# Performance work log

Measured on AMD Instinct MI355X. Metric: run time of the kernel, lower is better.

The kernel has to match this reference:

```python
import jax, jax.numpy as jnp
import numpy as np

B, D, E, H, OUT = 4096, 1024, 8, 4096, 1024


def setup_inputs() -> dict:
    key = jax.random.key(0)
    ks = jax.random.split(key, 8)
    s_in = 1.0 / np.sqrt(D)
    s_h = 1.0 / np.sqrt(H)
    return {
        "x": jax.random.normal(ks[0], (B, D), dtype=jnp.float32),
        "Wg": jax.random.uniform(ks[1], (D, E), minval=-s_in, maxval=s_in, dtype=jnp.float32),
        "bg": jnp.zeros((E,), dtype=jnp.float32),
        "W1": jax.random.uniform(ks[2], (E, D, H), minval=-s_in, maxval=s_in, dtype=jnp.float32),
        "b1": jnp.zeros((E, H), dtype=jnp.float32),
        "W2": jax.random.uniform(ks[3], (E, H, OUT), minval=-s_h, maxval=s_h, dtype=jnp.float32),
        "b2": jnp.zeros((E, OUT), dtype=jnp.float32),
        "w_bal": jnp.float32(0.01),
    }


def reference(x, Wg, bg, W1, b1, W2, b2, w_bal):
    # Gating: softmax then top-1 (== argmax of logits)
    gate_logits = x @ Wg + bg                      # [B, E]
    assign = jnp.argmax(gate_logits, axis=1)       # [B] top-1 expert
    onehot = jax.nn.one_hot(assign, E, dtype=x.dtype)  # [B, E] dispatch mask

    # Dense dispatch: run every expert MLP, combine by one-hot (top-1 select).
    # Original returns raw expert output (no gate-prob scaling).
    h = jax.nn.relu(jnp.einsum("bd,edh->ebh", x, W1) + b1[:, None, :])  # [E, B, H]
    y = jnp.einsum("ebh,eho->ebo", h, W2) + b2[:, None, :]              # [E, B, OUT]
    output = jnp.einsum("ebo,be->bo", y, onehot)                        # [B, OUT]

    # Load-balance loss on per-expert token counts
    loads = onehot.sum(axis=0)                     # [E]
    balance_loss = jnp.sum((loads - loads.mean()) ** 2) / E
    return output, balance_loss * w_bal
```

## Files before the change

kernel.cpp:

```cpp
#include <hip/hip_runtime.h>
#include <hip/hip_bf16.h>

typedef unsigned short u16;
typedef __attribute__((ext_vector_type(8))) short bf16x8;
typedef __attribute__((ext_vector_type(4))) float f32x4;

#define BTOK 4096
#define DDIM 1024
#define NEXP 8
#define HDIM 4096
#define ODIM 1024
#define MAXT 23
#define MROWS (MAXT * 256)

__device__ __forceinline__ u16 f2bf(float f) {
  unsigned u = __float_as_uint(f);
  return (u16)((u + 0x7FFFu + ((u >> 16) & 1u)) >> 16);
}
__device__ __forceinline__ u16 cvt_bf(float f) {
  __hip_bfloat16 h = __float2bfloat16(f);
  u16 r;
  __builtin_memcpy(&r, &h, 2);
  return r;
}

__device__ __forceinline__ void gload16(const void* g, void* l) {
  __builtin_amdgcn_global_load_lds(
      (const __attribute__((address_space(1))) void*)g,
      (__attribute__((address_space(3))) void*)l, 16, 0, 0);
}

__global__ __launch_bounds__(256) void init_kernel(int* __restrict__ ctrl,
                                                   int* __restrict__ rowmap) {
  int i = blockIdx.x * 256 + threadIdx.x;
  if (i < 1024)
    ctrl[i] = 0;
  else
    rowmap[i - 1024] = -1;
}

__global__ __launch_bounds__(256) void gate_kernel(
    const float* __restrict__ x, const float* __restrict__ Wg,
    const float* __restrict__ bg, int* __restrict__ assign,
    int* __restrict__ counts) {
  int wave = threadIdx.x >> 6;
  int lane = threadIdx.x & 63;
  int b = blockIdx.x * 4 + wave;
  const float* xr = x + (size_t)b * DDIM;
  double acc[NEXP];
#pragma unroll
  for (int e = 0; e < NEXP; ++e) acc[e] = 0.0;
  for (int d = lane; d < DDIM; d += 64) {
    float xv = xr[d];
    const float4* wrow = (const float4*)(Wg + d * NEXP);
    float4 w0 = wrow[0], w1 = wrow[1];
    acc[0] += (double)xv * (double)w0.x;
    acc[1] += (double)xv * (double)w0.y;
    acc[2] += (double)xv * (double)w0.z;
    acc[3] += (double)xv * (double)w0.w;
    acc[4] += (double)xv * (double)w1.x;
    acc[5] += (double)xv * (double)w1.y;
    acc[6] += (double)xv * (double)w1.z;
    acc[7] += (double)xv * (double)w1.w;
  }
#pragma unroll
  for (int e = 0; e < NEXP; ++e) {
    double v = acc[e];
#pragma unroll
    for (int off = 32; off > 0; off >>= 1) v += __shfl_xor(v, off);
    acc[e] = v;
  }
  if (lane == 0) {
    int best = 0;
    double bv = acc[0] + (double)bg[0];
#pragma unroll
    for (int e = 1; e < NEXP; ++e) {
      double v = acc[e] + (double)bg[e];
      if (v > bv) { bv = v; best = e; }
    }
    assign[b] = best;
    atomicAdd(&counts[best], 1);
  }
}

__global__ void setup_kernel(const int* __restrict__ counts,
                             const float* __restrict__ wbal,
                             int* __restrict__ offp, int* __restrict__ tile_e,
                             int* __restrict__ tile_m, int* __restrict__ meta,
                             float* __restrict__ loss_out) {
  if (threadIdx.x != 0 || blockIdx.x != 0) return;
  int off = 0, nt = 0;
  for (int e = 0; e < NEXP; ++e) {
    offp[e] = off;
    int pc = (counts[e] + 255) & ~255;
    for (int t = 0; t < (pc >> 8); ++t) {
      tile_e[nt] = e;
      tile_m[nt] = off + t * 256;
      ++nt;
    }
    off += pc;
  }
  offp[NEXP] = off;
  meta[0] = nt;
  float mean = (float)BTOK / (float)NEXP;
  float s = 0.f;
  for (int e = 0; e < NEXP; ++e) {
    float d = (float)counts[e] - mean;
    s += d * d;
  }
  loss_out[0] = s / (float)NEXP * wbal[0];
}

__global__ __launch_bounds__(256) void gather_kernel(
    const float* __restrict__ x, const int* __restrict__ assign,
    const int* __restrict__ offp, int* __restrict__ fill,
    int* __restrict__ rowmap, u16* __restrict__ xg) {
  int b = blockIdx.x;
  __shared__ int srow;
  if (threadIdx.x == 0) {
    int e = assign[b];
    int pos = atomicAdd(&fill[e], 1);
    int row = offp[e] + pos;
    rowmap[row] = b;
    srow = row;
  }
  __syncthreads();
  int row = srow;
  float4 v = *(const float4*)(x + (size_t)b * DDIM + threadIdx.x * 4);
  ushort4 o;
  o.x = f2bf(v.x);
  o.y = f2bf(v.y);
  o.z = f2bf(v.z);
  o.w = f2bf(v.w);
  *(ushort4*)(xg + (size_t)row * DDIM + threadIdx.x * 4) = o;
}

__global__ __launch_bounds__(256) void transpose_conv(
    const float* __restrict__ W, u16* __restrict__ wt, int N, int K) {
  const int e = blockIdx.z;
  const int kb = blockIdx.x * 128, nb = blockIdx.y * 64;
  __shared__ __align__(16) float lds[128][68];
  const float* src = W + (size_t)e * K * N;
  const int t = threadIdx.x;
  const int rr = t >> 4, cc = (t & 15) * 4;
#pragma unroll
  for (int p = 0; p < 8; ++p) {
    float4 v =
        *(const float4*)(src + (size_t)(kb + rr + p * 16) * N + nb + cc);
    *(float4*)&lds[rr + p * 16][cc] = v;
  }
  __syncthreads();
  const int n = t & 63, ks = (t >> 6) * 32;
  alignas(16) u16 tmp[32];
#pragma unroll
  for (int i = 0; i < 32; ++i) tmp[i] = cvt_bf(lds[ks + i][n]);
  u16* dst = wt + ((size_t)e * N + nb + n) * K + kb + ks;
  *(float4*)dst = *(float4*)&tmp[0];
  *(float4*)(dst + 8) = *(float4*)&tmp[8];
  *(float4*)(dst + 16) = *(float4*)&tmp[16];
  *(float4*)(dst + 24) = *(float4*)&tmp[24];
}

template <int MODE>
__device__ __forceinline__ void gemm_core(
    u16* lds, int bx, int by, int bz, const u16* __restrict__ A, int lda,
    const u16* __restrict__ BT, int ldb, int nbRows,
    const float* __restrict__ bias, const int* __restrict__ tile_e,
    const int* __restrict__ tile_m, u16* __restrict__ Hout, int ldn,
    float* __restrict__ P, size_t pStride, int nkt) {
  const int e = tile_e[bx];
  const int m0 = tile_m[bx];
  const int n0 = by * 128;
  const int kOff = bz * nkt * 32;

  const int tid = threadIdx.x;
  const int lane = tid & 63;
  const int wave = tid >> 6;
  const int wr = wave >> 1, wc = wave & 1;
  const int fr = lane & 15;
  const int kqr = lane >> 4;

  const int r0 = tid >> 2, k0 = (tid & 3) ^ ((r0 >> 1) & 3);
  const int r1 = (tid + 512) >> 2, k1 = ((tid + 512) & 3) ^ ((r1 >> 1) & 3);
  const u16* aS0 = A + (size_t)(m0 + r0) * lda + kOff + k0 * 8;
  const u16* aS1 = A + (size_t)(m0 + r1) * lda + kOff + k1 * 8;
  const u16* bPan = BT + ((size_t)e * nbRows + n0) * ldb + kOff;
  const u16* bS0 = bPan + (size_t)r0 * ldb + k0 * 8;
  const int dstA0 = (tid & ~63) * 8;
  const int dstA1 = dstA0 + 512 * 8;
  const int dstB = (tid & ~63) * 8;

  int aOff[4], bOff[4];
#pragma unroll
  for (int i = 0; i < 4; ++i) {
    int r = wr * 64 + i * 16 + fr;
    aOff[i] = (r * 4 + (kqr ^ ((r >> 1) & 3))) * 8;
    int c = wc * 64 + i * 16 + fr;
    bOff[i] = 8192 + (c * 4 + (kqr ^ ((c >> 1) & 3))) * 8;
  }

  f32x4 acc[4][4];
#pragma unroll
  for (int i = 0; i < 4; ++i)
#pragma unroll
    for (int j = 0; j < 4; ++j)
#pragma unroll
      for (int r = 0; r < 4; ++r) acc[i][j][r] = 0.f;

  auto stage = [&](int buf, int kt) {
    const int ko = kt * 32;
    u16* base = lds + buf * 12288;
    gload16(aS0 + ko, base + dstA0);
    gload16(aS1 + ko, base + dstA1);
    gload16(bS0 + ko, base + 8192 + dstB);
  };
  auto compute = [&](int buf) {
    const u16* base = lds + buf * 12288;
    bf16x8 af[4], bfr[4];
#pragma unroll
    for (int i = 0; i < 4; ++i) {
      af[i] = *(const bf16x8*)(base + aOff[i]);
      bfr[i] = *(const bf16x8*)(base + bOff[i]);
    }
    __builtin_amdgcn_s_setprio(1);
#pragma unroll
    for (int i = 0; i < 4; ++i)
#pragma unroll
      for (int j = 0; j < 4; ++j)
        acc[i][j] = __builtin_amdgcn_mfma_f32_16x16x32_bf16(af[i], bfr[j],
                                                            acc[i][j], 0, 0, 0);
    __builtin_amdgcn_s_setprio(0);
  };

  stage(0, 0);
  stage(1, 1);
  __builtin_amdgcn_sched_barrier(0);
  asm volatile("s_waitcnt vmcnt(3)" ::: "memory");
  __builtin_amdgcn_s_barrier();
  __builtin_amdgcn_sched_barrier(0);

  int cur = 0, nst = 2;
#pragma unroll 1
  for (int t = 0; t < nkt; ++t) {
    const bool more = (t + 2 < nkt);
    if (more) stage(nst, t + 2);
    compute(cur);
    cur = (cur == 2) ? 0 : cur + 1;
    nst = (nst == 2) ? 0 : nst + 1;
    if (t + 1 < nkt) {
      __builtin_amdgcn_sched_barrier(0);
      if (more)
        asm volatile("s_waitcnt vmcnt(3)" ::: "memory");
      else
        asm volatile("s_waitcnt vmcnt(0)" ::: "memory");
      __builtin_amdgcn_s_barrier();
      __builtin_amdgcn_sched_barrier(0);
    }
  }

  if constexpr (MODE == 0) {
#pragma unroll
    for (int i = 0; i < 4; ++i) {
      int rbase = m0 + wr * 64 + i * 16 + (lane >> 4) * 4;
#pragma unroll
      for (int j = 0; j < 4; ++j) {
        int col = n0 + wc * 64 + j * 16 + fr;
        float bv = bias[e * ldn + col];
#pragma unroll
        for (int r = 0; r < 4; ++r) {
          float v = acc[i][j][r] + bv;
          v = v > 0.f ? v : 0.f;
          Hout[(size_t)(rbase + r) * ldn + col] = f2bf(v);
        }
      }
    }
  } else {
    float* Pp = P + bz * pStride;
#pragma unroll
    for (int i = 0; i < 4; ++i) {
      int rbase = m0 + wr * 64 + i * 16 + (lane >> 4) * 4;
#pragma unroll
      for (int j = 0; j < 4; ++j) {
        int col = n0 + wc * 64 + j * 16 + fr;
#pragma unroll
        for (int r = 0; r < 4; ++r)
          Pp[(size_t)(rbase + r) * ODIM + col] = acc[i][j][r];
      }
    }
  }
}

__global__ __launch_bounds__(512, 4) void moe_gemm1(
    const u16* __restrict__ xg, const u16* __restrict__ wt1,
    const float* __restrict__ b1, const int* __restrict__ tile_e,
    const int* __restrict__ tile_m, const int* __restrict__ meta,
    u16* __restrict__ h) {
  __shared__ __align__(16) u16 lds[3 * 12288];
  const int orig = blockIdx.y * MAXT + blockIdx.x;
  const int xcd = orig & 7;
  const int i = orig >> 3;
  const int bx = i >> 2;
  const int by = xcd * 4 + (i & 3);
  if (bx >= meta[0]) return;
  gemm_core<0>(lds, bx, by, 0, xg, DDIM, wt1, DDIM, HDIM, b1, tile_e, tile_m,
               h, HDIM, nullptr, 0, DDIM / 32);
}

__global__ __launch_bounds__(512, 4) void moe_gemm2(
    const u16* __restrict__ h, const u16* __restrict__ wt2,
    const int* __restrict__ tile_e, const int* __restrict__ tile_m,
    const int* __restrict__ meta, float* __restrict__ P, size_t pStride) {
  __shared__ __align__(16) u16 lds[3 * 12288];
  const int orig = blockIdx.y * MAXT + blockIdx.x;
  const int xcd = orig & 7;
  const int i = orig >> 3;
  const int bx = i;
  const int by = xcd;
  if (bx >= meta[0]) return;
  gemm_core<1>(lds, bx, by, blockIdx.z, h, HDIM, wt2, HDIM, ODIM, nullptr,
               tile_e, tile_m, nullptr, 0, P, pStride, (HDIM / 2) / 32);
}

__global__ __launch_bounds__(256) void reduce_kernel(
    const float* __restrict__ P, size_t pStride, const int* __restrict__ rowmap,
    const int* __restrict__ tile_e, const int* __restrict__ tile_m,
    const int* __restrict__ meta, const float* __restrict__ b2,
    float* __restrict__ out) {
  if ((int)blockIdx.x >= meta[0]) return;
  const int e = tile_e[blockIdx.x];
  const int m0 = tile_m[blockIdx.x];
  const int c0 = blockIdx.y * 128;
#pragma unroll 1
  for (int it = 0; it < 32; ++it) {
    int idx = it * 256 + threadIdx.x;
    int r = idx >> 5, cq = idx & 31;
    int row = m0 + r;
    int tok = rowmap[row];
    if (tok < 0) continue;
    int c = c0 + cq * 4;
    float4 a = *(const float4*)(P + (size_t)row * ODIM + c);
    float4 b = *(const float4*)(P + pStride + (size_t)row * ODIM + c);
    float4 bb = *(const float4*)(b2 + (size_t)e * ODIM + c);
    float4 o;
    o.x = a.x + b.x + bb.x;
    o.y = a.y + b.y + bb.y;
    o.z = a.z + b.z + bb.z;
    o.w = a.w + b.w + bb.w;
    *(float4*)(out + (size_t)tok * ODIM + c) = o;
  }
}

extern "C" void kernel_launch(void* const* d_in, const int* in_sizes, int n_in,
                              void* d_out, int out_size, void* d_ws,
                              size_t ws_size, hipStream_t stream) {
  const float* x = (const float*)d_in[0];
  const float* Wg = (const float*)d_in[1];
  const float* bg = (const float*)d_in[2];
  const float* W1 = (const float*)d_in[3];
  const float* b1 = (const float*)d_in[4];
  const float* W2 = (const float*)d_in[5];
  const float* b2 = (const float*)d_in[6];
  const float* wbal = (const float*)d_in[7];
  float* out = (float*)d_out;

  char* ws = (char*)d_ws;
  int* counts = (int*)(ws + 0);
  int* fill = (int*)(ws + 64);
  int* offp = (int*)(ws + 128);
  int* meta = (int*)(ws + 192);
  int* tile_e = (int*)(ws + 256);
  int* tile_m = (int*)(ws + 512);
  int* assign = (int*)(ws + 4096);
  int* rowmap = (int*)(ws + 20480);
  u16* xg = (u16*)(ws + 65536);
  u16* h = (u16*)(ws + 12582912);
  float* P = (float*)(ws + 61865984);
  u16* wt1 = (u16*)(ws + 110100480);
  u16* wt2 = (u16*)(ws + 177209344);
  const size_t pStride = (size_t)MROWS * ODIM;

  init_kernel<<<27, 256, 0, stream>>>((int*)ws, rowmap);
  gate_kernel<<<BTOK / 4, 256, 0, stream>>>(x, Wg, bg, assign, counts);
  setup_kernel<<<1, 64, 0, stream>>>(counts, wbal, offp, tile_e, tile_m, meta,
                                     out + (size_t)BTOK * ODIM);
  gather_kernel<<<BTOK, 256, 0, stream>>>(x, assign, offp, fill, rowmap, xg);

  transpose_conv<<<dim3(DDIM / 128, HDIM / 64, NEXP), 256, 0, stream>>>(
      W1, wt1, HDIM, DDIM);
  transpose_conv<<<dim3(HDIM / 128, ODIM / 64, NEXP), 256, 0, stream>>>(
      W2, wt2, ODIM, HDIM);

  moe_gemm1<<<dim3(MAXT, HDIM / 128), 512, 0, stream>>>(
      xg, wt1, b1, tile_e, tile_m, meta, h);
  moe_gemm2<<<dim3(MAXT, ODIM / 128, 2), 512, 0, stream>>>(
      h, wt2, tile_e, tile_m, meta, P, pStride);
  reduce_kernel<<<dim3(MAXT, ODIM / 128), 256, 0, stream>>>(
      P, pStride, rowmap, tile_e, tile_m, meta, b2, out);
}
```

Baseline: 374.9 us.

## Rewrite grouped GEMMs as 256x256 tiles with 8-phase ping-pong LDS schedule

Replaces the 128x128 triple-buffered GEMM core with a 256x256 tile, BK=64 kernel. It uses double-buffered 64KB LDS halves and an interleaved schedule of partial loads, barriers and MFMA quadrants, so global-to-LDS copies overlap with compute at finer granularity. It also remaps the grid for XCD locality and widens the transpose_conv tile to 256 rows. The change aims to raise arithmetic intensity and hide load latency, at the cost of lower occupancy (2 blocks per CU, 128KB LDS), more register pressure, and coarser tiles that waste work on padded expert tiles.

```diff
diff --git a/kernel.cpp b/kernel.cpp
--- a/kernel.cpp
+++ b/kernel.cpp
@@ -23,12 +23,19 @@
   __builtin_memcpy(&r, &h, 2);
   return r;
 }
-
 __device__ __forceinline__ void gload16(const void* g, void* l) {
   __builtin_amdgcn_global_load_lds(
       (const __attribute__((address_space(1))) void*)g,
       (__attribute__((address_space(3))) void*)l, 16, 0, 0);
 }
+
+#define SFENCE __builtin_amdgcn_sched_barrier(0)
+#define SBAR                        \
+  do {                              \
+    SFENCE;                         \
+    __builtin_amdgcn_s_barrier();   \
+    SFENCE;                         \
+  } while (0)
 
 __global__ __launch_bounds__(256) void init_kernel(int* __restrict__ ctrl,
                                                    int* __restrict__ rowmap) {
@@ -138,187 +145,255 @@
 __global__ __launch_bounds__(256) void transpose_conv(
     const float* __restrict__ W, u16* __restrict__ wt, int N, int K) {
   const int e = blockIdx.z;
-  const int kb = blockIdx.x * 128, nb = blockIdx.y * 64;
-  __shared__ __align__(16) float lds[128][68];
+  const int kb = blockIdx.x * 256, nb = blockIdx.y * 64;
+  __shared__ __align__(16) float lds[256][66];
   const float* src = W + (size_t)e * K * N;
   const int t = threadIdx.x;
   const int rr = t >> 4, cc = (t & 15) * 4;
 #pragma unroll
-  for (int p = 0; p < 8; ++p) {
+  for (int p = 0; p < 16; ++p) {
     float4 v =
         *(const float4*)(src + (size_t)(kb + rr + p * 16) * N + nb + cc);
     *(float4*)&lds[rr + p * 16][cc] = v;
   }
   __syncthreads();
-  const int n = t & 63, ks = (t >> 6) * 32;
-  alignas(16) u16 tmp[32];
-#pragma unroll
-  for (int i = 0; i < 32; ++i) tmp[i] = cvt_bf(lds[ks + i][n]);
-  u16* dst = wt + ((size_t)e * N + nb + n) * K + kb + ks;
-  *(float4*)dst = *(float4*)&tmp[0];
-  *(float4*)(dst + 8) = *(float4*)&tmp[8];
-  *(float4*)(dst + 16) = *(float4*)&tmp[16];
-  *(float4*)(dst + 24) = *(float4*)&tmp[24];
+  const int n = t & 63, kg = (t >> 6) * 64;
+  alignas(16) u16 tmp[64];
+#pragma unroll
+  for (int i = 0; i < 64; ++i) tmp[i] = cvt_bf(lds[kg + i][n]);
+  u16* dst = wt + ((size_t)e * N + nb + n) * K + kb + kg;
+#pragma unroll
+  for (int q = 0; q < 8; ++q) *(float4*)(dst + q * 8) = *(float4*)&tmp[q * 8];
 }
 
 template <int MODE>
-__device__ __forceinline__ void gemm_core(
-    u16* lds, int bx, int by, int bz, const u16* __restrict__ A, int lda,
+__device__ __forceinline__ void gemm8p_core(
+    char* lds, int bx, int by, int bz, const u16* __restrict__ A, int lda,
     const u16* __restrict__ BT, int ldb, int nbRows,
     const float* __restrict__ bias, const int* __restrict__ tile_e,
     const int* __restrict__ tile_m, u16* __restrict__ Hout, int ldn,
-    float* __restrict__ P, size_t pStride, int nkt) {
+    float* __restrict__ P, size_t pStride, int NT, int kOff) {
   const int e = tile_e[bx];
   const int m0 = tile_m[bx];
-  const int n0 = by * 128;
-  const int kOff = bz * nkt * 32;
+  const int n0 = by * 256;
 
   const int tid = threadIdx.x;
   const int lane = tid & 63;
-  const int wave = tid >> 6;
-  const int wr = wave >> 1, wc = wave & 1;
+  const int wid = tid >> 6;
+  const int wr = wid >> 2;
+  const int wc = wid & 3;
   const int fr = lane & 15;
   const int kqr = lane >> 4;
 
-  const int r0 = tid >> 2, k0 = (tid & 3) ^ ((r0 >> 1) & 3);
-  const int r1 = (tid + 512) >> 2, k1 = ((tid + 512) & 3) ^ ((r1 >> 1) & 3);
-  const u16* aS0 = A + (size_t)(m0 + r0) * lda + kOff + k0 * 8;
-  const u16* aS1 = A + (size_t)(m0 + r1) * lda + kOff + k1 * 8;
-  const u16* bPan = BT + ((size_t)e * nbRows + n0) * ldb + kOff;
-  const u16* bS0 = bPan + (size_t)r0 * ldb + k0 * 8;
-  const int dstA0 = (tid & ~63) * 8;
-  const int dstA1 = dstA0 + 512 * 8;
-  const int dstB = (tid & ~63) * 8;
-
-  int aOff[4], bOff[4];
-#pragma unroll
-  for (int i = 0; i < 4; ++i) {
-    int r = wr * 64 + i * 16 + fr;
-    aOff[i] = (r * 4 + (kqr ^ ((r >> 1) & 3))) * 8;
-    int c = wc * 64 + i * 16 + fr;
-    bOff[i] = 8192 + (c * 4 + (kqr ^ ((c >> 1) & 3))) * 8;
-  }
-
-  f32x4 acc[4][4];
-#pragma unroll
-  for (int i = 0; i < 4; ++i)
+  const int rS = tid >> 3, gS = tid & 7;
+  const int koctOff = (gS ^ (rS & 7)) * 8;
+  const u16* aB0 = A + (size_t)(m0 + rS) * lda + kOff + koctOff;
+  const u16* bB0 = BT + ((size_t)e * nbRows + n0 + rS) * ldb + kOff + koctOff;
+
+  auto stageA = [&](int kt, int half) {
+    char* dst = lds + (kt & 1) * 65536 + half * 16384 + tid * 16;
+    const u16* s = aB0 + (size_t)(half * 128) * lda + kt * 64;
+    gload16(s, dst);
+    gload16(s + (size_t)64 * lda, dst + 8192);
+  };
+  auto stageB = [&](int kt, int half) {
+    char* dst = lds + (kt & 1) * 65536 + 32768 + half * 16384 + tid * 16;
+    const u16* s = bB0 + (size_t)(half * 128) * ldb + kt * 64;
+    gload16(s, dst);
+    gload16(s + (size_t)64 * ldb, dst + 8192);
+  };
+
+  int aOff[4][2], bOff[2][2];
+#pragma unroll
+  for (int mi = 0; mi < 4; ++mi) {
+    int r = wr * 64 + mi * 16 + fr;
+#pragma unroll
+    for (int ks = 0; ks < 2; ++ks)
+      aOff[mi][ks] = r * 128 + (((ks * 4 + kqr) ^ (r & 7)) * 16);
+  }
+#pragma unroll
+  for (int ni = 0; ni < 2; ++ni) {
+    int c = wc * 32 + ni * 16 + fr;
+#pragma unroll
+    for (int ks = 0; ks < 2; ++ks)
+      bOff[ni][ks] = c * 128 + (((ks * 4 + kqr) ^ (c & 7)) * 16);
+  }
+
+  f32x4 acc[8][4];
+#pragma unroll
+  for (int i = 0; i < 8; ++i)
 #pragma unroll
     for (int j = 0; j < 4; ++j)
 #pragma unroll
       for (int r = 0; r < 4; ++r) acc[i][j][r] = 0.f;
 
-  auto stage = [&](int buf, int kt) {
-    const int ko = kt * 32;
-    u16* base = lds + buf * 12288;
-    gload16(aS0 + ko, base + dstA0);
-    gload16(aS1 + ko, base + dstA1);
-    gload16(bS0 + ko, base + 8192 + dstB);
+  bf16x8 af[4][2], bA[2][2], bB[2][2];
+
+  auto ldA = [&](int dB, int mq) {
+    const char* rg = lds + dB + mq * 16384;
+#pragma unroll
+    for (int mi = 0; mi < 4; ++mi)
+#pragma unroll
+      for (int ks = 0; ks < 2; ++ks)
+        af[mi][ks] = *(const bf16x8*)(rg + aOff[mi][ks]);
   };
-  auto compute = [&](int buf) {
-    const u16* base = lds + buf * 12288;
-    bf16x8 af[4], bfr[4];
-#pragma unroll
-    for (int i = 0; i < 4; ++i) {
-      af[i] = *(const bf16x8*)(base + aOff[i]);
-      bfr[i] = *(const bf16x8*)(base + bOff[i]);
-    }
+  auto ldB = [&](int dB, int nq, bf16x8 (&bf)[2][2]) {
+    const char* rg = lds + dB + 32768 + nq * 16384;
+#pragma unroll
+    for (int ni = 0; ni < 2; ++ni)
+#pragma unroll
+      for (int ks = 0; ks < 2; ++ks)
+        bf[ni][ks] = *(const bf16x8*)(rg + bOff[ni][ks]);
+  };
+  auto MM = [&](int mq, int nq, bf16x8 (&bf)[2][2]) {
     __builtin_amdgcn_s_setprio(1);
 #pragma unroll
-    for (int i = 0; i < 4; ++i)
-#pragma unroll
-      for (int j = 0; j < 4; ++j)
-        acc[i][j] = __builtin_amdgcn_mfma_f32_16x16x32_bf16(af[i], bfr[j],
-                                                            acc[i][j], 0, 0, 0);
+    for (int ks = 0; ks < 2; ++ks)
+#pragma unroll
+      for (int mi = 0; mi < 4; ++mi)
+#pragma unroll
+        for (int ni = 0; ni < 2; ++ni)
+          acc[mq * 4 + mi][nq * 2 + ni] = __builtin_amdgcn_mfma_f32_16x16x32_bf16(
+              af[mi][ks], bf[ni][ks], acc[mq * 4 + mi][nq * 2 + ni], 0, 0, 0);
     __builtin_amdgcn_s_setprio(0);
   };
 
-  stage(0, 0);
-  stage(1, 1);
-  __builtin_amdgcn_sched_barrier(0);
-  asm volatile("s_waitcnt vmcnt(3)" ::: "memory");
-  __builtin_amdgcn_s_barrier();
-  __builtin_amdgcn_sched_barrier(0);
-
-  int cur = 0, nst = 2;
+  stageA(0, 0);
+  stageB(0, 0);
+  stageA(0, 1);
+  stageB(0, 1);
+  stageA(1, 0);
+  stageB(1, 0);
+  asm volatile("s_waitcnt vmcnt(8)" ::: "memory");
+  SBAR;
+
+  const int NI = NT >> 1;
 #pragma unroll 1
-  for (int t = 0; t < nkt; ++t) {
-    const bool more = (t + 2 < nkt);
-    if (more) stage(nst, t + 2);
-    compute(cur);
-    cur = (cur == 2) ? 0 : cur + 1;
-    nst = (nst == 2) ? 0 : nst + 1;
-    if (t + 1 < nkt) {
-      __builtin_amdgcn_sched_barrier(0);
-      if (more)
-        asm volatile("s_waitcnt vmcnt(3)" ::: "memory");
-      else
-        asm volatile("s_waitcnt vmcnt(0)" ::: "memory");
-      __builtin_amdgcn_s_barrier();
-      __builtin_amdgcn_sched_barrier(0);
+  for (int i = 0; i < NI; ++i) {
+    const int kt1 = 2 * i + 1, kt2 = 2 * i + 2, kt3 = 2 * i + 3;
+    const bool more = (i + 1 < NI);
+    ldA(0, 0);
+    ldB(0, 0, bA);
+    stageA(kt1, 1);
+    SBAR;
+    asm volatile("s_waitcnt lgkmcnt(0)" ::: "memory");
+    SFENCE;
+    MM(0, 0, bA);
+    asm volatile("s_waitcnt vmcnt(6)" ::: "memory");
+    SBAR;
+    ldB(0, 1, bB);
+    stageB(kt1, 1);
+    SBAR;
+    asm volatile("s_waitcnt lgkmcnt(0)" ::: "memory");
+    SFENCE;
+    MM(0, 1, bB);
+    SBAR;
+    ldA(0, 1);
+    if (more) stageA(kt2, 0);
+    SBAR;
+    asm volatile("s_waitcnt lgkmcnt(0)" ::: "memory");
+    SFENCE;
+    MM(1, 0, bA);
+    SBAR;
+    if (more) stageB(kt2, 0);
+    SBAR;
+    MM(1, 1, bB);
+    if (more)
+      asm volatile("s_waitcnt vmcnt(8)" ::: "memory");
+    else
+      asm volatile("s_waitcnt vmcnt(0)" ::: "memory");
+    SBAR;
+    ldA(65536, 0);
+    ldB(65536, 0, bA);
+    if (more) stageA(kt2, 1);
+    SBAR;
+    asm volatile("s_waitcnt lgkmcnt(0)" ::: "memory");
+    SFENCE;
+    MM(0, 0, bA);
+    if (more) asm volatile("s_waitcnt vmcnt(6)" ::: "memory");
+    SBAR;
+    ldB(65536, 1, bB);
+    if (more) stageB(kt2, 1);
+    SBAR;
+    asm volatile("s_waitcnt lgkmcnt(0)" ::: "memory");
+    SFENCE;
+    MM(0, 1, bB);
+    SBAR;
+    ldA(65536, 1);
+    if (more) stageA(kt3, 0);
+    SBAR;
+    asm volatile("s_waitcnt lgkmcnt(0)" ::: "memory");
+    SFENCE;
+    MM(1, 0, bA);
+    SBAR;
+    if (more) stageB(kt3, 0);
+    SBAR;
+    MM(1, 1, bB);
+    if (more) asm volatile("s_waitcnt vmcnt(8)" ::: "memory");
+    SBAR;
+  }
+
+#pragma unroll
+  for (int mq = 0; mq < 2; ++mq)
+#pragma unroll
+    for (int mi = 0; mi < 4; ++mi) {
+      const int rbase = m0 + mq * 128 + wr * 64 + mi * 16 + (lane >> 4) * 4;
+#pragma unroll
+      for (int nq = 0; nq < 2; ++nq)
+#pragma unroll
+        for (int ni = 0; ni < 2; ++ni) {
+          const int col = n0 + nq * 128 + wc * 32 + ni * 16 + fr;
+          const f32x4 a = acc[mq * 4 + mi][nq * 2 + ni];
+          if constexpr (MODE == 0) {
+            const float bv = bias[e * ldn + col];
+#pragma unroll
+            for (int r = 0; r < 4; ++r) {
+              float v = a[r] + bv;
+              v = v > 0.f ? v : 0.f;
+              Hout[(size_t)(rbase + r) * ldn + col] = f2bf(v);
+            }
+          } else {
+            float* Pp = P + bz * pStride;
+#pragma unroll
+            for (int r = 0; r < 4; ++r)
+              Pp[(size_t)(rbase + r) * ODIM + col] = a[r];
+          }
+        }
     }
-  }
-
-  if constexpr (MODE == 0) {
-#pragma unroll
-    for (int i = 0; i < 4; ++i) {
-      int rbase = m0 + wr * 64 + i * 16 + (lane >> 4) * 4;
-#pragma unroll
-      for (int j = 0; j < 4; ++j) {
-        int col = n0 + wc * 64 + j * 16 + fr;
-        float bv = bias[e * ldn + col];
-#pragma unroll
-        for (int r = 0; r < 4; ++r) {
-          float v = acc[i][j][r] + bv;
-          v = v > 0.f ? v : 0.f;
-          Hout[(size_t)(rbase + r) * ldn + col] = f2bf(v);
-        }
-      }
-    }
-  } else {
-    float* Pp = P + bz * pStride;
-#pragma unroll
-    for (int i = 0; i < 4; ++i) {
-      int rbase = m0 + wr * 64 + i * 16 + (lane >> 4) * 4;
-#pragma unroll
-      for (int j = 0; j < 4; ++j) {
-        int col = n0 + wc * 64 + j * 16 + fr;
-#pragma unroll
-        for (int r = 0; r < 4; ++r)
-          Pp[(size_t)(rbase + r) * ODIM + col] = acc[i][j][r];
-      }
-    }
-  }
-}
-
-__global__ __launch_bounds__(512, 4) void moe_gemm1(
+}
+
+__global__ __launch_bounds__(512, 2) void moe_gemm1(
     const u16* __restrict__ xg, const u16* __restrict__ wt1,
     const float* __restrict__ b1, const int* __restrict__ tile_e,
     const int* __restrict__ tile_m, const int* __restrict__ meta,
     u16* __restrict__ h) {
-  __shared__ __align__(16) u16 lds[3 * 12288];
+  __shared__ __align__(16) char lds[131072];
   const int orig = blockIdx.y * MAXT + blockIdx.x;
   const int xcd = orig & 7;
-  const int i = orig >> 3;
-  const int bx = i >> 2;
-  const int by = xcd * 4 + (i & 3);
+  const int idx = orig >> 3;
+  const int by = xcd * 2 + idx / MAXT;
+  const int bx = idx % MAXT;
   if (bx >= meta[0]) return;
-  gemm_core<0>(lds, bx, by, 0, xg, DDIM, wt1, DDIM, HDIM, b1, tile_e, tile_m,
-               h, HDIM, nullptr, 0, DDIM / 32);
-}
-
-__global__ __launch_bounds__(512, 4) void moe_gemm2(
+  gemm8p_core<0>(lds, bx, by, 0, xg, DDIM, wt1, DDIM, HDIM, b1, tile_e,
+                 tile_m, h, HDIM, nullptr, 0, DDIM / 64, 0);
+}
+
+__global__ __launch_bounds__(512, 2) void moe_gemm2(
     const u16* __restrict__ h, const u16* __restrict__ wt2,
     const int* __restrict__ tile_e, const int* __restrict__ tile_m,
     const int* __restrict__ meta, float* __restrict__ P, size_t pStride) {
-  __shared__ __align__(16) u16 lds[3 * 12288];
-  const int orig = blockIdx.y * MAXT + blockIdx.x;
+  __shared__ __align__(16) char lds[131072];
+  const int orig = (blockIdx.z * 4 + blockIdx.y) * MAXT + blockIdx.x;
   const int xcd = orig & 7;
-  const int i = orig >> 3;
-  const int bx = i;
-  const int by = xcd;
+  const int idx = orig >> 3;
+  const int wg = xcd * MAXT + idx;
+  const int z = wg / 92;
+  const int rem = wg % 92;
+  const int by = rem / MAXT;
+  const int bx = rem % MAXT;
   if (bx >= meta[0]) return;
-  gemm_core<1>(lds, bx, by, blockIdx.z, h, HDIM, wt2, HDIM, ODIM, nullptr,
-               tile_e, tile_m, nullptr, 0, P, pStride, (HDIM / 2) / 32);
+  gemm8p_core<1>(lds, bx, by, z, h, HDIM, wt2, HDIM, ODIM, nullptr, tile_e,
+                 tile_m, nullptr, 0, P, pStride, 32, z * 2048);
 }
 
 __global__ __launch_bounds__(256) void reduce_kernel(
@@ -385,14 +460,14 @@
                                      out + (size_t)BTOK * ODIM);
   gather_kernel<<<BTOK, 256, 0, stream>>>(x, assign, offp, fill, rowmap, xg);
 
-  transpose_conv<<<dim3(DDIM / 128, HDIM / 64, NEXP), 256, 0, stream>>>(
+  transpose_conv<<<dim3(DDIM / 256, HDIM / 64, NEXP), 256, 0, stream>>>(
       W1, wt1, HDIM, DDIM);
-  transpose_conv<<<dim3(HDIM / 128, ODIM / 64, NEXP), 256, 0, stream>>>(
+  transpose_conv<<<dim3(HDIM / 256, ODIM / 64, NEXP), 256, 0, stream>>>(
       W2, wt2, ODIM, HDIM);
 
-  moe_gemm1<<<dim3(MAXT, HDIM / 128), 512, 0, stream>>>(
+  moe_gemm1<<<dim3(MAXT, HDIM / 256), 512, 0, stream>>>(
       xg, wt1, b1, tile_e, tile_m, meta, h);
-  moe_gemm2<<<dim3(MAXT, ODIM / 128, 2), 512, 0, stream>>>(
+  moe_gemm2<<<dim3(MAXT, ODIM / 256, 2), 512, 0, stream>>>(
       h, wt2, tile_e, tile_m, meta, P, pStride);
   reduce_kernel<<<dim3(MAXT, ODIM / 128), 256, 0, stream>>>(
       P, pStride, rowmap, tile_e, tile_m, meta, b2, out);
```

After: 352.4 us, median of 3. 1.06x faster.
